# Kernel tuning notes

Measured on AMD Instinct MI355X. Metric: run time of the kernel, lower is better.

The kernel has to match this reference:

```python
import jax, jax.numpy as jnp
import numpy as np

ALPHA = 0.2  # LeakyReLU negative slope
MASK_VAL = -9e15


def setup_inputs() -> dict:
    key = jax.random.key(0)
    k1, k2, k3, k4 = jax.random.split(key, 4)
    N, F_in, F_out = 8192, 512, 128
    h = jax.random.normal(k1, (N, F_in), dtype=jnp.float32)
    adj = jax.random.randint(k2, (N, N), 0, 2, dtype=jnp.int32)
    w = jax.random.normal(k3, (F_in, F_out), dtype=jnp.float32) * 0.05
    a = jax.random.normal(k4, (2 * F_out, 1), dtype=jnp.float32) * 0.05
    return {"h": h, "adj": adj, "w": w, "a": a}


def reference(h, adj, w, a):
    F_out = w.shape[1]
    Wh = h @ w                                  # [N, F_out]
    Wh1 = Wh @ a[:F_out, :]                     # [N, 1]
    Wh2 = Wh @ a[F_out:, :]                     # [N, 1]
    e = Wh1 + Wh2.T                             # [N, N] broadcast additive score
    e = jnp.where(e > 0, e, ALPHA * e)          # LeakyReLU
    att = jnp.where(adj > 0, e, MASK_VAL)       # mask non-edges
    att = jax.nn.softmax(att, axis=1)           # row softmax
    # dropout is identity in eval mode
    h_prime = att @ Wh                          # [N, F_out]
    return jax.nn.elu(h_prime)                  # concat=True -> ELU
```

## Files before the change

### kernel.cpp

```cpp
#include <hip/hip_runtime.h>
#include <hip/hip_bf16.h>

#define LRELU_ALPHA 0.2f

constexpr int N   = 8192;
constexpr int FIN = 512;
constexpr int F   = 128;
constexpr int BRW = 16;
constexpr int BR  = 64;

typedef __attribute__((ext_vector_type(4))) float f32x4;
typedef __attribute__((ext_vector_type(8))) short s16x8;
typedef unsigned long long u64;

static __device__ __forceinline__ short f2bf(float x) {
  unsigned u = __float_as_uint(x);
  return (short)((u + 0x7fffu + ((u >> 16) & 1u)) >> 16);
}

__global__ __launch_bounds__(512) void k_wh(
    const float* __restrict__ h, const float* __restrict__ w,
    const float* __restrict__ a, short* __restrict__ Bpack,
    float* __restrict__ Wh1, float* __restrict__ Wh2) {
  __shared__ float hl[32][68];
  __shared__ float wl[64][128];
  const int t    = threadIdx.x;
  const int i0   = blockIdx.x * 32;
  const int col4 = (t & 31) * 4;
  const int rq   = t >> 5;
  float acc[2][4] = {};

  for (int k0 = 0; k0 < FIN; k0 += 64) {
    *(f32x4*)&hl[t >> 4][(t & 15) * 4] =
        *(const f32x4*)(h + (size_t)(i0 + (t >> 4)) * FIN + k0 + (t & 15) * 4);
#pragma unroll
    for (int j = 0; j < 4; ++j) {
      int c = t + 512 * j;
      int kr = c >> 5, f4 = (c & 31) * 4;
      *(f32x4*)&wl[kr][f4] = *(const f32x4*)(w + (size_t)(k0 + kr) * F + f4);
    }
    __syncthreads();
#pragma unroll 4
    for (int k4 = 0; k4 < 64; k4 += 4) {
      f32x4 wv[4];
#pragma unroll
      for (int u = 0; u < 4; ++u) wv[u] = *(const f32x4*)&wl[k4 + u][col4];
#pragma unroll
      for (int ri = 0; ri < 2; ++ri) {
        f32x4 hv = *(const f32x4*)&hl[rq * 2 + ri][k4];
#pragma unroll
        for (int u = 0; u < 4; ++u) {
#pragma unroll
          for (int ci = 0; ci < 4; ++ci) acc[ri][ci] += hv[u] * wv[u][ci];
        }
      }
    }
    __syncthreads();
  }
  {
    const int kt    = blockIdx.x;
    const int kslot = rq >> 2;
    const int u     = (rq * 2) & 7;
#pragma unroll
    for (int ci = 0; ci < 4; ++ci) {
      int f = col4 + ci;
      int nb = f >> 4, c = f & 15;
      unsigned pk = (unsigned)(unsigned short)f2bf(acc[0][ci]) |
                    ((unsigned)(unsigned short)f2bf(acc[1][ci]) << 16);
      size_t idx = (size_t)(kt * 8 + nb) * 512 + (kslot * 16 + c) * 8 + u;
      *(unsigned*)(Bpack + idx) = pk;
    }
  }
  f32x4 av1 = *(const f32x4*)(a + col4);
  f32x4 av2 = *(const f32x4*)(a + F + col4);
  float s1[2], s2[2];
#pragma unroll
  for (int ri = 0; ri < 2; ++ri) {
    s1[ri] = acc[ri][0] * av1[0] + acc[ri][1] * av1[1] +
             acc[ri][2] * av1[2] + acc[ri][3] * av1[3];
    s2[ri] = acc[ri][0] * av2[0] + acc[ri][1] * av2[1] +
             acc[ri][2] * av2[2] + acc[ri][3] * av2[3];
  }
#pragma unroll
  for (int off = 1; off < 32; off <<= 1) {
#pragma unroll
    for (int ri = 0; ri < 2; ++ri) {
      s1[ri] += __shfl_xor(s1[ri], off);
      s2[ri] += __shfl_xor(s2[ri], off);
    }
  }
  if ((t & 31) == 0) {
#pragma unroll
    for (int ri = 0; ri < 2; ++ri) {
      Wh1[i0 + rq * 2 + ri] = s1[ri];
      Wh2[i0 + rq * 2 + ri] = s2[ri];
    }
  }
}

template <int KS>
__global__ __launch_bounds__(256) void k_attn(
    const int* __restrict__ adj, const float* __restrict__ Wh1v,
    const float* __restrict__ Wh2v, const short* __restrict__ Bpack,
    float* __restrict__ accP, float* __restrict__ lP) {
  constexpr int JW  = N / KS;
  constexpr int NTL = JW / 32;
  __shared__ float w2l[JW];

  const int t   = threadIdx.x;
  const int l   = t & 63;
  const int w   = t >> 6;
  const int r16 = l & 15;
  const int g8  = (l >> 4) * 8;
  const int q2  = l >> 5;
  const int j32 = l & 31;
  const int i0  = blockIdx.x * BR;
  const int s   = blockIdx.y;

  const int row  = i0 + w * BRW + r16;
  const float w1 = Wh1v[row];
  const int* __restrict__ rp = adj + (size_t)(i0 + w * BRW) * N +
                               (size_t)s * JW;
  const short* __restrict__ bq = Bpack + (size_t)s * NTL * 8 * 512 + l * 8;

  f32x4 acc[8] = {};
  float lsum = 0.f;
  int adjA[8], adjB[8];
  s16x8 bfA[8], bfB[8];

#define ADJ_LOAD(vv, tt)                                                     \
  _Pragma("unroll") for (int i = 0; i < 8; ++i)                              \
      vv[i] = rp[(size_t)(2 * i + q2) * N + (tt) * 32 + j32];
#define BF_LOAD(bf, tt)                                                      \
  _Pragma("unroll") for (int nb = 0; nb < 8; ++nb)                           \
      bf[nb] = *(const s16x8*)(bq + (size_t)((tt) * 8 + nb) * 512);

  auto mask_byte = [&](const int (&vv)[8]) -> unsigned {
    const unsigned sh = (unsigned)((r16 & 1) * 32 + g8);
    unsigned byte = 0;
#pragma unroll
    for (int i = 0; i < 8; ++i) {
      u64 m = __ballot(vv[i] > 0);
      unsigned b = (unsigned)(m >> sh) & 0xffu;
      byte = ((r16 >> 1) == i) ? b : byte;
    }
    return byte;
  };

  auto scores8 = [&](unsigned mb, int tt, s16x8& af) {
    const f32x4 y0 = *(const f32x4*)&w2l[tt * 32 + g8];
    const f32x4 y1 = *(const f32x4*)&w2l[tt * 32 + g8 + 4];
    float p[8];
#pragma unroll
    for (int u = 0; u < 4; ++u) {
      float x = w1 + y0[u]; x = fmaxf(x, LRELU_ALPHA * x);
      p[u] = (mb >> u) & 1u ? __expf(x) : 0.f;
    }
#pragma unroll
    for (int u = 0; u < 4; ++u) {
      float x = w1 + y1[u]; x = fmaxf(x, LRELU_ALPHA * x);
      p[4 + u] = (mb >> (4 + u)) & 1u ? __expf(x) : 0.f;
    }
#pragma unroll
    for (int u = 0; u < 8; ++u) lsum += p[u];
    af = s16x8{f2bf(p[0]), f2bf(p[1]), f2bf(p[2]), f2bf(p[3]),
               f2bf(p[4]), f2bf(p[5]), f2bf(p[6]), f2bf(p[7])};
  };

#pragma unroll
  for (int j4 = t; j4 < JW / 4; j4 += 256)
    *(f32x4*)&w2l[j4 * 4] = *(const f32x4*)(Wh2v + (size_t)s * JW + j4 * 4);
  ADJ_LOAD(adjA, 0)
  BF_LOAD(bfA, 0)
  ADJ_LOAD(adjB, 1)
  __syncthreads();

  for (int tt = 0; tt < NTL; tt += 2) {
    {
      BF_LOAD(bfB, tt + 1)
      unsigned mb = mask_byte(adjA);
      if (tt + 2 < NTL) ADJ_LOAD(adjA, tt + 2)
      s16x8 af;
      scores8(mb, tt, af);
#pragma unroll
      for (int nb = 0; nb < 8; ++nb)
        acc[nb] = __builtin_amdgcn_mfma_f32_16x16x32_bf16(af, bfA[nb],
                                                          acc[nb], 0, 0, 0);
    }
    {
      if (tt + 2 < NTL) BF_LOAD(bfA, tt + 2)
      unsigned mb = mask_byte(adjB);
      if (tt + 3 < NTL) ADJ_LOAD(adjB, tt + 3)
      s16x8 af;
      scores8(mb, tt + 1, af);
#pragma unroll
      for (int nb = 0; nb < 8; ++nb)
        acc[nb] = __builtin_amdgcn_mfma_f32_16x16x32_bf16(af, bfB[nb],
                                                          acc[nb], 0, 0, 0);
    }
  }
#undef ADJ_LOAD
#undef BF_LOAD

  lsum += __shfl_xor(lsum, 16);
  lsum += __shfl_xor(lsum, 32);
  if (l < 16) lP[(size_t)s * N + row] = lsum;
  float* op = accP + (size_t)s * N * F;
#pragma unroll
  for (int nb = 0; nb < 8; ++nb) {
#pragma unroll
    for (int rg = 0; rg < 4; ++rg) {
      int r = i0 + w * BRW + (l >> 4) * 4 + rg;
      op[(size_t)r * F + nb * 16 + r16] = acc[nb][rg];
    }
  }
}

template <int KS>
__global__ __launch_bounds__(256) void k_comb(
    const float* __restrict__ accP, const float* __restrict__ lP,
    float* __restrict__ out) {
  const int idx = blockIdx.x * 256 + threadIdx.x;
  const int i   = idx >> 5;
  f32x4 v = {};
  float lt = 0.f;
#pragma unroll
  for (int s = 0; s < KS; ++s) {
    v += *(const f32x4*)(accP + (size_t)s * N * F + (size_t)idx * 4);
    lt += lP[(size_t)s * N + i];
  }
  f32x4 o;
#pragma unroll
  for (int u = 0; u < 4; ++u) {
    float x = v[u] / lt;
    o[u] = x > 0.f ? x : __expf(x) - 1.f;
  }
  *(f32x4*)(out + (size_t)idx * 4) = o;
}

extern "C" void kernel_launch(void* const* d_in, const int* in_sizes, int n_in,
                              void* d_out, int out_size, void* d_ws, size_t ws_size,
                              hipStream_t stream) {
  const float* h   = (const float*)d_in[0];
  const int*   adj = (const int*)d_in[1];
  const float* w   = (const float*)d_in[2];
  const float* a   = (const float*)d_in[3];
  float* out = (float*)d_out;

  char* ws = (char*)d_ws;
  short* Bpack = (short*)ws;
  float* Wh1 = (float*)(ws + (size_t)F * N * 2);
  float* Wh2 = Wh1 + N;
  float* lP  = Wh2 + N;

  const size_t fixed = (size_t)F * N * 2 + 2 * (size_t)N * 4;
  const size_t need8 = fixed + 8 * (size_t)N * 4 + 8 * (size_t)N * F * 4;

  k_wh<<<N / 32, 512, 0, stream>>>(h, w, a, Bpack, Wh1, Wh2);
  if (ws_size >= need8) {
    constexpr int KS = 8;
    float* accP = lP + (size_t)KS * N;
    k_attn<KS><<<dim3(N / BR, KS), 256, 0, stream>>>(adj, Wh1, Wh2, Bpack,
                                                     accP, lP);
    k_comb<KS><<<(N * F / 4) / 256, 256, 0, stream>>>(accP, lP, out);
  } else {
    constexpr int KS = 4;
    float* accP = lP + (size_t)KS * N;
    k_attn<KS><<<dim3(N / BR, KS), 256, 0, stream>>>(adj, Wh1, Wh2, Bpack,
                                                     accP, lP);
    k_comb<KS><<<(N * F / 4) / 256, 256, 0, stream>>>(accP, lP, out);
  }
}
```

Baseline: 143.4 us.

## Precompute adjacency bitmask in the projection kernel and stream bits into attention

The first kernel now interleaves extra blocks that read the int32 adjacency matrix and ballot it into a packed 64-bit bitmask per row, written to the workspace. The attention kernel reads one u64 per row per 64 columns instead of int32 adjacency values, which removes the per-tile ballot/select logic and most of its global-load traffic. The adjacency is still read once, plus a small extra mask write and read, and a waves-per-EU hint is added to the attention kernel. It also makes the workspace larger, which may change whether the KS=8 path is chosen.

```diff
diff --git a/kernel.cpp b/kernel.cpp
--- a/kernel.cpp
+++ b/kernel.cpp
@@ -18,14 +18,40 @@
   return (short)((u + 0x7fffu + ((u >> 16) & 1u)) >> 16);
 }
 
-__global__ __launch_bounds__(512) void k_wh(
+__global__ __launch_bounds__(512) void k_prod(
     const float* __restrict__ h, const float* __restrict__ w,
-    const float* __restrict__ a, short* __restrict__ Bpack,
-    float* __restrict__ Wh1, float* __restrict__ Wh2) {
+    const float* __restrict__ a, const int* __restrict__ adj,
+    short* __restrict__ Bpack, float* __restrict__ Wh1,
+    float* __restrict__ Wh2, u64* __restrict__ mask) {
+  const int bx = blockIdx.x;
+  if ((bx % 5) != 4) {
+    const int mask_id = (bx / 5) * 4 + (bx % 5);
+    const int l   = threadIdx.x & 63;
+    const int row = mask_id * 8 + (threadIdx.x >> 6);
+    const int* __restrict__ rp = adj + (size_t)row * N;
+    u64* __restrict__ mp = mask + (size_t)row * (N / 64);
+    for (int it = 0; it < N / 512; ++it) {
+      int v[8];
+#pragma unroll
+      for (int k = 0; k < 8; ++k) v[k] = rp[it * 512 + l + k * 64];
+      u64 m[8];
+#pragma unroll
+      for (int k = 0; k < 8; ++k) m[k] = __ballot(v[k] > 0);
+      if (l == 0) {
+        ulonglong2 s0 = {m[0], m[1]}, s1 = {m[2], m[3]};
+        ulonglong2 s2 = {m[4], m[5]}, s3 = {m[6], m[7]};
+        *(ulonglong2*)(mp + it * 8)     = s0;
+        *(ulonglong2*)(mp + it * 8 + 2) = s1;
+        *(ulonglong2*)(mp + it * 8 + 4) = s2;
+        *(ulonglong2*)(mp + it * 8 + 6) = s3;
+      }
+    }
+    return;
+  }
   __shared__ float hl[32][68];
   __shared__ float wl[64][128];
   const int t    = threadIdx.x;
-  const int i0   = blockIdx.x * 32;
+  const int i0   = (bx / 5) * 32;
   const int col4 = (t & 31) * 4;
   const int rq   = t >> 5;
   float acc[2][4] = {};
@@ -58,7 +84,7 @@
     __syncthreads();
   }
   {
-    const int kt    = blockIdx.x;
+    const int kt    = i0 >> 5;
     const int kslot = rq >> 2;
     const int u     = (rq * 2) & 7;
 #pragma unroll
@@ -99,8 +125,9 @@
 }
 
 template <int KS>
-__global__ __launch_bounds__(256) void k_attn(
-    const int* __restrict__ adj, const float* __restrict__ Wh1v,
+__global__ __launch_bounds__(256) __attribute__((amdgpu_waves_per_eu(1, 4)))
+void k_attn(
+    const u64* __restrict__ mask, const float* __restrict__ Wh1v,
     const float* __restrict__ Wh2v, const short* __restrict__ Bpack,
     float* __restrict__ accP, float* __restrict__ lP) {
   constexpr int JW  = N / KS;
@@ -112,40 +139,22 @@
   const int w   = t >> 6;
   const int r16 = l & 15;
   const int g8  = (l >> 4) * 8;
-  const int q2  = l >> 5;
-  const int j32 = l & 31;
   const int i0  = blockIdx.x * BR;
   const int s   = blockIdx.y;
 
   const int row  = i0 + w * BRW + r16;
   const float w1 = Wh1v[row];
-  const int* __restrict__ rp = adj + (size_t)(i0 + w * BRW) * N +
-                               (size_t)s * JW;
+  const u64* __restrict__ mrow = mask + (size_t)row * (N / 64) + s * (JW / 64);
   const short* __restrict__ bq = Bpack + (size_t)s * NTL * 8 * 512 + l * 8;
 
   f32x4 acc[8] = {};
   float lsum = 0.f;
-  int adjA[8], adjB[8];
   s16x8 bfA[8], bfB[8];
-
-#define ADJ_LOAD(vv, tt)                                                     \
-  _Pragma("unroll") for (int i = 0; i < 8; ++i)                              \
-      vv[i] = rp[(size_t)(2 * i + q2) * N + (tt) * 32 + j32];
+  u64 mA, mB;
+
 #define BF_LOAD(bf, tt)                                                      \
   _Pragma("unroll") for (int nb = 0; nb < 8; ++nb)                           \
       bf[nb] = *(const s16x8*)(bq + (size_t)((tt) * 8 + nb) * 512);
-
-  auto mask_byte = [&](const int (&vv)[8]) -> unsigned {
-    const unsigned sh = (unsigned)((r16 & 1) * 32 + g8);
-    unsigned byte = 0;
-#pragma unroll
-    for (int i = 0; i < 8; ++i) {
-      u64 m = __ballot(vv[i] > 0);
-      unsigned b = (unsigned)(m >> sh) & 0xffu;
-      byte = ((r16 >> 1) == i) ? b : byte;
-    }
-    return byte;
-  };
 
   auto scores8 = [&](unsigned mb, int tt, s16x8& af) {
     const f32x4 y0 = *(const f32x4*)&w2l[tt * 32 + g8];
@@ -170,18 +179,16 @@
 #pragma unroll
   for (int j4 = t; j4 < JW / 4; j4 += 256)
     *(f32x4*)&w2l[j4 * 4] = *(const f32x4*)(Wh2v + (size_t)s * JW + j4 * 4);
-  ADJ_LOAD(adjA, 0)
   BF_LOAD(bfA, 0)
-  ADJ_LOAD(adjB, 1)
+  mA = mrow[0];
   __syncthreads();
 
   for (int tt = 0; tt < NTL; tt += 2) {
     {
       BF_LOAD(bfB, tt + 1)
-      unsigned mb = mask_byte(adjA);
-      if (tt + 2 < NTL) ADJ_LOAD(adjA, tt + 2)
+      if (tt + 2 < NTL) mB = mrow[tt / 2 + 1];
       s16x8 af;
-      scores8(mb, tt, af);
+      scores8((unsigned)(mA >> g8) & 0xffu, tt, af);
 #pragma unroll
       for (int nb = 0; nb < 8; ++nb)
         acc[nb] = __builtin_amdgcn_mfma_f32_16x16x32_bf16(af, bfA[nb],
@@ -189,17 +196,15 @@
     }
     {
       if (tt + 2 < NTL) BF_LOAD(bfA, tt + 2)
-      unsigned mb = mask_byte(adjB);
-      if (tt + 3 < NTL) ADJ_LOAD(adjB, tt + 3)
       s16x8 af;
-      scores8(mb, tt + 1, af);
+      scores8((unsigned)(mA >> (32 + g8)) & 0xffu, tt + 1, af);
 #pragma unroll
       for (int nb = 0; nb < 8; ++nb)
         acc[nb] = __builtin_amdgcn_mfma_f32_16x16x32_bf16(af, bfB[nb],
                                                           acc[nb], 0, 0, 0);
-    }
-  }
-#undef ADJ_LOAD
+      mA = mB;
+    }
+  }
 #undef BF_LOAD
 
   lsum += __shfl_xor(lsum, 16);
@@ -251,22 +256,24 @@
   short* Bpack = (short*)ws;
   float* Wh1 = (float*)(ws + (size_t)F * N * 2);
   float* Wh2 = Wh1 + N;
-  float* lP  = Wh2 + N;
-
-  const size_t fixed = (size_t)F * N * 2 + 2 * (size_t)N * 4;
+  u64*  mask = (u64*)(Wh2 + N);
+  float* lP  = (float*)(mask + (size_t)N * (N / 64));
+
+  const size_t fixed = (size_t)F * N * 2 + 2 * (size_t)N * 4 +
+                       (size_t)N * (N / 64) * 8;
   const size_t need8 = fixed + 8 * (size_t)N * 4 + 8 * (size_t)N * F * 4;
 
-  k_wh<<<N / 32, 512, 0, stream>>>(h, w, a, Bpack, Wh1, Wh2);
+  k_prod<<<1280, 512, 0, stream>>>(h, w, a, adj, Bpack, Wh1, Wh2, mask);
   if (ws_size >= need8) {
     constexpr int KS = 8;
     float* accP = lP + (size_t)KS * N;
-    k_attn<KS><<<dim3(N / BR, KS), 256, 0, stream>>>(adj, Wh1, Wh2, Bpack,
+    k_attn<KS><<<dim3(N / BR, KS), 256, 0, stream>>>(mask, Wh1, Wh2, Bpack,
                                                      accP, lP);
     k_comb<KS><<<(N * F / 4) / 256, 256, 0, stream>>>(accP, lP, out);
   } else {
     constexpr int KS = 4;
     float* accP = lP + (size_t)KS * N;
-    k_attn<KS><<<dim3(N / BR, KS), 256, 0, stream>>>(adj, Wh1, Wh2, Bpack,
+    k_attn<KS><<<dim3(N / BR, KS), 256, 0, stream>>>(mask, Wh1, Wh2, Bpack,
                                                      accP, lP);
     k_comb<KS><<<(N * F / 4) / 256, 256, 0, stream>>>(accP, lP, out);
   }
```

Result: faster. 137.3 us (-4.2%).
